# Performance work log

Measured on AMD Instinct MI355X. Metric: run time of the kernel, lower is better.

The kernel has to match this reference:

```python
import jax, jax.numpy as jnp
import numpy as np

N, E, G = 50000, 800000, 128
H, NUM_RBF, CUTOFF, TIME_DIM, L = 128, 32, 6.0, 64, 4
MAX_Z, LIGAND_NODE = 128, 1
M_IN = 3 * H + NUM_RBF + 1


def _ln(x, g, b, eps=1e-5):
    mu = x.mean(-1, keepdims=True)
    var = ((x - mu) ** 2).mean(-1, keepdims=True)
    return (x - mu) * jax.lax.rsqrt(var + eps) * g + b


def _sin_emb(t, dim):
    half = dim // 2
    freqs = jnp.exp(jnp.arange(half, dtype=jnp.float32) * (-np.log(10000.0) / (half - 1)))
    args = t[:, None] * freqs[None, :]
    return jnp.concatenate([jnp.sin(args), jnp.cos(args)], axis=-1)


def setup_inputs() -> dict:
    key = jax.random.key(0)
    ks = jax.random.split(key, 32)
    d = {}
    d['z'] = jax.random.randint(ks[0], (N,), 0, MAX_Z)
    d['node_type'] = jax.random.randint(ks[1], (N,), 0, 2)
    d['pos'] = jax.random.normal(ks[2], (N, 3), jnp.float32) * 3.0
    d['edge_index'] = jax.random.randint(ks[3], (2, E), 0, N)
    d['edge_type'] = jax.random.randint(ks[4], (E,), 0, 2)
    d['batch'] = jnp.sort(jax.random.randint(ks[5], (N,), 0, G))
    d['t'] = jax.random.uniform(ks[6], (G,), jnp.float32)

    def lin(k, fi, fo):
        return jax.random.normal(k, (fi, fo), jnp.float32) / np.sqrt(fi)

    d['emb_z'] = jax.random.normal(ks[7], (MAX_Z, H), jnp.float32) * 0.02
    d['emb_nt'] = jax.random.normal(ks[8], (2, H), jnp.float32) * 0.02
    d['in_norm_g'] = jnp.ones((H,), jnp.float32)
    d['in_norm_b'] = jnp.zeros((H,), jnp.float32)
    d['time_w1'] = lin(ks[9], TIME_DIM, H); d['time_b1'] = jnp.zeros((H,), jnp.float32)
    d['time_w2'] = lin(ks[10], H, H); d['time_b2'] = jnp.zeros((H,), jnp.float32)
    d['l_edge_emb'] = jax.random.normal(ks[11], (L, 2, H), jnp.float32) * 0.02
    d['l_msg_w1'] = jax.random.normal(ks[12], (L, M_IN, H), jnp.float32) / np.sqrt(M_IN)
    d['l_msg_b1'] = jnp.zeros((L, H), jnp.float32)
    d['l_msg_w2'] = jax.random.normal(ks[13], (L, H, H), jnp.float32) / np.sqrt(H)
    d['l_msg_b2'] = jnp.zeros((L, H), jnp.float32)
    d['l_upd_w1'] = jax.random.normal(ks[14], (L, 2 * H, H), jnp.float32) / np.sqrt(2 * H)
    d['l_upd_b1'] = jnp.zeros((L, H), jnp.float32)
    d['l_upd_w2'] = jax.random.normal(ks[15], (L, H, H), jnp.float32) / np.sqrt(H)
    d['l_upd_b2'] = jnp.zeros((L, H), jnp.float32)
    d['l_norm_g'] = jnp.ones((L, H), jnp.float32)
    d['l_norm_b'] = jnp.zeros((L, H), jnp.float32)
    d['head_w1'] = lin(ks[16], H, H); d['head_b1'] = jnp.zeros((H,), jnp.float32)
    d['head_w2'] = lin(ks[17], H, 1); d['head_b2'] = jnp.zeros((1,), jnp.float32)
    return d


def reference(z, node_type, pos, edge_index, edge_type, batch, t,
              emb_z, emb_nt, in_norm_g, in_norm_b,
              time_w1, time_b1, time_w2, time_b2,
              l_edge_emb, l_msg_w1, l_msg_b1, l_msg_w2, l_msg_b2,
              l_upd_w1, l_upd_b1, l_upd_w2, l_upd_b2, l_norm_g, l_norm_b,
              head_w1, head_b1, head_w2, head_b2):
    centers = jnp.linspace(0.0, CUTOFF, NUM_RBF)
    step = CUTOFF / (NUM_RBF - 1)
    gamma = 1.0 / max(step * step, 1e-6)

    h = emb_z[jnp.clip(z, 0, MAX_Z - 1)] + emb_nt[node_type]
    tf = jax.nn.silu(_sin_emb(t, TIME_DIM) @ time_w1 + time_b1) @ time_w2 + time_b2
    h = h + tf[batch]
    h = _ln(h, in_norm_g, in_norm_b)

    src, dst = edge_index[0], edge_index[1]
    rel = pos[src] - pos[dst]                     # [E,3]
    dist = jnp.linalg.norm(rel, axis=-1)          # [E]
    radial = jnp.exp(-gamma * (dist[:, None] - centers[None, :]) ** 2)  # [E,R]
    lig = node_type == LIGAND_NODE

    for i in range(L):
        ek = l_edge_emb[i][edge_type]             # [E,H]
        m_in = jnp.concatenate([h[src], h[dst], ek, radial, dist[:, None]], axis=-1)
        msg = jax.nn.silu(m_in @ l_msg_w1[i] + l_msg_b1[i])
        msg = jax.nn.silu(msg @ l_msg_w2[i] + l_msg_b2[i])
        sums = jax.ops.segment_sum(msg, dst, num_segments=N)
        cnt = jax.ops.segment_sum(jnp.ones((E,), h.dtype), dst, num_segments=N)
        agg = sums / jnp.clip(cnt, 1.0)[:, None]
        upd = jax.nn.silu(jnp.concatenate([h, agg], axis=-1) @ l_upd_w1[i] + l_upd_b1[i])
        upd = upd @ l_upd_w2[i] + l_upd_b2[i]
        h = jnp.where(lig[:, None], _ln(h + upd, l_norm_g[i], l_norm_b[i]), h)

    mask = lig.astype(h.dtype)
    gsum = jax.ops.segment_sum(h * mask[:, None], batch, num_segments=G)
    gcnt = jax.ops.segment_sum(mask, batch, num_segments=G)
    gf = gsum / jnp.clip(gcnt, 1.0)[:, None]
    out = jax.nn.silu(gf @ head_w1 + head_b1) @ head_w2 + head_b2
    return out.squeeze(-1)
```

## Files before the change

### kernel.cpp

```cpp
#include <hip/hip_runtime.h>
#include <hip/hip_bf16.h>

#define NN 50000
#define EE 800000
#define GG 128
#define HH 128

typedef __bf16 bf16;
typedef __attribute__((ext_vector_type(8))) __bf16 bf16x8;
typedef __attribute__((ext_vector_type(4))) float f32x4;

__device__ __forceinline__ float silu_f(float x) { return x / (1.0f + __expf(-x)); }

__global__ void prep_weights(const float* __restrict__ w1, const float* __restrict__ w2,
                             const float* __restrict__ u1, const float* __restrict__ u2,
                             const float* __restrict__ ee, const float* __restrict__ mb1,
                             bf16* __restrict__ W1abt, bf16* __restrict__ W1rt,
                             bf16* __restrict__ W2t, bf16* __restrict__ U1t,
                             bf16* __restrict__ U2t) {
    int idx = blockIdx.x * 256 + threadIdx.x;
    if (idx < 131072) {
        int l = idx >> 15, rem = idx & 32767;
        int c = rem >> 7, k = rem & 127;
        int krow = k + ((c >= 128) ? 128 : 0);
        W1abt[idx] = (bf16)w1[(size_t)l * 417 * 128 + (size_t)krow * 128 + (c & 127)];
    } else if ((idx -= 131072) < 32768) {
        int l = idx >> 13, rem = idx & 8191;
        int c = rem >> 6, k = rem & 63;
        const float* w1l = w1 + (size_t)l * 417 * 128;
        float v = 0.0f;
        if (k < 32) v = w1l[(size_t)(384 + k) * 128 + c];
        else if (k == 32) v = w1l[(size_t)416 * 128 + c];
        else if (k == 33) {
            v = mb1[l * 128 + c];
            for (int t = 0; t < 128; ++t)
                v += ee[(size_t)l * 256 + t] * w1l[(size_t)(256 + t) * 128 + c];
        } else if (k == 34) {
            for (int t = 0; t < 128; ++t)
                v += (ee[(size_t)l * 256 + 128 + t] - ee[(size_t)l * 256 + t]) *
                     w1l[(size_t)(256 + t) * 128 + c];
        }
        W1rt[idx] = (bf16)v;
    } else if ((idx -= 32768) < 65536) {
        int l = idx / 16384, rem = idx % 16384;
        int n = rem / 128, k = rem % 128;
        W2t[idx] = (bf16)w2[(size_t)l * 16384 + (size_t)k * 128 + n];
    } else if ((idx -= 65536) < 131072) {
        int l = idx / 32768, rem = idx % 32768;
        int n = rem / 256, k = rem % 256;
        U1t[idx] = (bf16)u1[(size_t)l * 32768 + (size_t)k * 128 + n];
    } else if ((idx -= 131072) < 65536) {
        int l = idx / 16384, rem = idx % 16384;
        int n = rem / 128, k = rem % 128;
        U2t[idx] = (bf16)u2[(size_t)l * 16384 + (size_t)k * 128 + n];
    }
}

__global__ void time_mlp(const float* __restrict__ t, const float* __restrict__ w1,
                         const float* __restrict__ b1, const float* __restrict__ w2,
                         const float* __restrict__ b2, float* __restrict__ tf) {
    int g = blockIdx.x, c = threadIdx.x;
    __shared__ float sL[64], uT[128];
    float tv = t[g];
    if (c < 32) {
        float fr = expf(-(float)c * (logf(10000.0f) / 31.0f));
        float arg = tv * fr;
        sL[c] = sinf(arg);
        sL[c + 32] = cosf(arg);
    }
    __syncthreads();
    float acc = b1[c];
    for (int k = 0; k < 64; ++k) acc += sL[k] * w1[k * 128 + c];
    uT[c] = silu_f(acc);
    __syncthreads();
    float acc2 = b2[c];
    for (int k = 0; k < 128; ++k) acc2 += uT[k] * w2[k * 128 + c];
    tf[g * 128 + c] = acc2;
}

__global__ void node_init(const int* __restrict__ z, const int* __restrict__ nt,
                          const int* __restrict__ batch, const float* __restrict__ tf,
                          const float* __restrict__ emb_z, const float* __restrict__ emb_nt,
                          const float* __restrict__ g, const float* __restrict__ b,
                          float* __restrict__ hg, bf16* __restrict__ hb) {
    int n = blockIdx.x, c = threadIdx.x;
    __shared__ float red[128];
    int zz = min(max(z[n], 0), 127);
    float v = emb_z[zz * 128 + c] + emb_nt[nt[n] * 128 + c] + tf[batch[n] * 128 + c];
    red[c] = v;
    __syncthreads();
    for (int s = 64; s > 0; s >>= 1) { if (c < s) red[c] += red[c + s]; __syncthreads(); }
    float mu = red[0] * (1.0f / 128.0f);
    __syncthreads();
    float dv = v - mu;
    red[c] = dv * dv;
    __syncthreads();
    for (int s = 64; s > 0; s >>= 1) { if (c < s) red[c] += red[c + s]; __syncthreads(); }
    float var = red[0] * (1.0f / 128.0f);
    float o = dv * rsqrtf(var + 1e-5f) * g[c] + b[c];
    hg[(size_t)n * 128 + c] = o;
    hb[(size_t)n * 128 + c] = (bf16)o;
}

__global__ void edge_pre(const int* __restrict__ ei, const float* __restrict__ pos,
                         float* __restrict__ dist_raw, int* __restrict__ cnt) {
    int e = blockIdx.x * 256 + threadIdx.x;
    if (e >= EE) return;
    int s = ei[e], d = ei[EE + e];
    float dx = pos[s * 3 + 0] - pos[d * 3 + 0];
    float dy = pos[s * 3 + 1] - pos[d * 3 + 1];
    float dz = pos[s * 3 + 2] - pos[d * 3 + 2];
    dist_raw[e] = sqrtf(dx * dx + dy * dy + dz * dz);
    atomicAdd(&cnt[d], 1);
}

__global__ void scan_kernel(const int* __restrict__ cnt, int* __restrict__ cursor) {
    __shared__ int part[1024];
    int t = threadIdx.x;
    const int per = (NN + 1023) / 1024;
    int start = t * per, end = min(start + per, NN);
    int s = 0;
    for (int i = start; i < end; ++i) s += cnt[i];
    part[t] = s;
    __syncthreads();
    for (int off = 1; off < 1024; off <<= 1) {
        int v = (t >= off) ? part[t - off] : 0;
        __syncthreads();
        part[t] += v;
        __syncthreads();
    }
    int base = (t == 0) ? 0 : part[t - 1];
    for (int i = start; i < end; ++i) { cursor[i] = base; base += cnt[i]; }
}

__global__ void scatter_kernel(const int* __restrict__ ei, const int* __restrict__ et,
                               const float* __restrict__ dist_raw, int* __restrict__ cursor,
                               int* __restrict__ src_s, int* __restrict__ dst_s,
                               int* __restrict__ type_s, float* __restrict__ dist_s) {
    int e = blockIdx.x * 256 + threadIdx.x;
    if (e >= EE) return;
    int d = ei[EE + e];
    int p = atomicAdd(&cursor[d], 1);
    src_s[p] = ei[e];
    dst_s[p] = d;
    type_s[p] = et[e];
    dist_s[p] = dist_raw[e];
}

__global__ __launch_bounds__(256) void node_pre(
    const bf16* __restrict__ hb, const bf16* __restrict__ W1abt,
    float* __restrict__ Xs, float* __restrict__ Xd) {
    __shared__ bf16 xL[64 * 128];
    const int tid = threadIdx.x;
    const int lane = tid & 63, wave = tid >> 6;
    const int wr = wave >> 1, wc = wave & 1;
    const int lrow = lane & 15, lgrp = lane >> 4;
    const int nb0 = blockIdx.x * 64;
    const int r0 = wr * 32 + lrow, r1 = r0 + 16;

    for (int i = tid; i < 64 * 16; i += 256) {
        const int row = i >> 4, cc = i & 15;
        const int node = nb0 + row;
        bf16x8 v;
        if (node < NN) v = *(const bf16x8*)(hb + (size_t)node * 128 + cc * 8);
        else { for (int j = 0; j < 8; ++j) v[j] = (bf16)0.0f; }
        *(bf16x8*)(xL + row * 128 + ((cc ^ (row & 15)) * 8)) = v;
    }
    __syncthreads();

    f32x4 acc[2][8] = {};
    for (int ks = 0; ks < 4; ++ks) {
        const int cb = ks * 4 + lgrp;
        bf16x8 a0 = *(const bf16x8*)(xL + r0 * 128 + ((cb ^ (r0 & 15)) * 8));
        bf16x8 a1 = *(const bf16x8*)(xL + r1 * 128 + ((cb ^ (r1 & 15)) * 8));
        const int k0 = ks * 32 + lgrp * 8;
#pragma unroll
        for (int ni = 0; ni < 8; ++ni) {
            const int col = wc * 128 + ni * 16 + lrow;
            bf16x8 b = *(const bf16x8*)(W1abt + (size_t)col * 128 + k0);
            acc[0][ni] = __builtin_amdgcn_mfma_f32_16x16x32_bf16(a0, b, acc[0][ni], 0, 0, 0);
            acc[1][ni] = __builtin_amdgcn_mfma_f32_16x16x32_bf16(a1, b, acc[1][ni], 0, 0, 0);
        }
    }
#pragma unroll
    for (int mi = 0; mi < 2; ++mi) {
#pragma unroll
        for (int r = 0; r < 4; ++r) {
            const int row = wr * 32 + mi * 16 + lgrp * 4 + r;
            const int node = nb0 + row;
            if (node >= NN) continue;
#pragma unroll
            for (int ni = 0; ni < 8; ++ni) {
                const int col = wc * 128 + ni * 16 + lrow;
                float v = (mi == 0 ? acc[0][ni][r] : acc[1][ni][r]);
                if (col < 128) Xs[(size_t)node * 128 + col] = v;
                else Xd[(size_t)node * 128 + (col - 128)] = v;
            }
        }
    }
}

__global__ __launch_bounds__(256) void edge_kernel(
    const int* __restrict__ src_s, const int* __restrict__ dst_s,
    const int* __restrict__ type_s, const float* __restrict__ dist_s,
    const float* __restrict__ Xs, const float* __restrict__ Xd,
    const bf16* __restrict__ W1rt, const bf16* __restrict__ W2t,
    const float* __restrict__ b2, float* __restrict__ sums) {
    __shared__ bf16 msgL[64 * 128];
    __shared__ int dstL[64];
    __shared__ int srcL[64];
    const int tid = threadIdx.x;
    const int lane = tid & 63, wave = tid >> 6;
    const int wr = wave >> 1, wc = wave & 1;
    const int lrow = lane & 15, lgrp = lane >> 4;
    const int eb = blockIdx.x * 64;

    const int r0 = wr * 32 + lrow;
    const int r1 = r0 + 16;
    const int e0 = eb + r0, e1 = eb + r1;
    const int ty0 = type_s[e0], ty1 = type_s[e1];
    const float di0 = dist_s[e0], di1 = dist_s[e1];
    if (tid < 64) { dstL[tid] = dst_s[eb + tid]; srcL[tid] = src_s[eb + tid]; }
    __syncthreads();

    const float step = 6.0f / 31.0f;
    const float gamma = 1.0f / (step * step);

    f32x4 acc[2][4] = {};
#pragma unroll
    for (int ks = 0; ks < 2; ++ks) {
        const int k0 = ks * 32 + lgrp * 8;
        bf16x8 a0, a1;
        if (k0 < 32) {
#pragma unroll
            for (int j = 0; j < 8; ++j) {
                float cj = (float)(k0 + j) * step;
                float v0 = di0 - cj, v1 = di1 - cj;
                a0[j] = (bf16)__expf(-gamma * v0 * v0);
                a1[j] = (bf16)__expf(-gamma * v1 * v1);
            }
        } else {
#pragma unroll
            for (int j = 0; j < 8; ++j) { a0[j] = (bf16)0.0f; a1[j] = (bf16)0.0f; }
            if (k0 == 32) {
                a0[0] = (bf16)di0; a1[0] = (bf16)di1;
                a0[1] = (bf16)1.0f; a1[1] = (bf16)1.0f;
                a0[2] = (bf16)(float)ty0; a1[2] = (bf16)(float)ty1;
            }
        }
#pragma unroll
        for (int ni = 0; ni < 4; ++ni) {
            const int col = wc * 64 + ni * 16 + lrow;
            bf16x8 b = *(const bf16x8*)(W1rt + (size_t)col * 64 + k0);
            acc[0][ni] = __builtin_amdgcn_mfma_f32_16x16x32_bf16(a0, b, acc[0][ni], 0, 0, 0);
            acc[1][ni] = __builtin_amdgcn_mfma_f32_16x16x32_bf16(a1, b, acc[1][ni], 0, 0, 0);
        }
    }
#pragma unroll
    for (int mi = 0; mi < 2; ++mi) {
#pragma unroll
        for (int r = 0; r < 4; ++r) {
            const int row = wr * 32 + mi * 16 + lgrp * 4 + r;
            const int sn = srcL[row], dn = dstL[row];
            const float* xs = Xs + (size_t)sn * 128;
            const float* xd = Xd + (size_t)dn * 128;
#pragma unroll
            for (int ni = 0; ni < 4; ++ni) {
                const int col = wc * 64 + ni * 16 + lrow;
                float v = (mi == 0 ? acc[0][ni][r] : acc[1][ni][r]) + xs[col] + xd[col];
                v = silu_f(v);
                const int cc = col >> 3;
                msgL[row * 128 + ((cc ^ (row & 15)) * 8) + (col & 7)] = (bf16)v;
            }
        }
    }
    __syncthreads();

    f32x4 acc2[2][4] = {};
#pragma unroll
    for (int ks = 0; ks < 4; ++ks) {
        const int cb = ks * 4 + lgrp;
        bf16x8 a0 = *(const bf16x8*)(msgL + r0 * 128 + ((cb ^ (r0 & 15)) * 8));
        bf16x8 a1 = *(const bf16x8*)(msgL + r1 * 128 + ((cb ^ (r1 & 15)) * 8));
        const int k0 = ks * 32 + lgrp * 8;
#pragma unroll
        for (int ni = 0; ni < 4; ++ni) {
            const int col = wc * 64 + ni * 16 + lrow;
            bf16x8 b = *(const bf16x8*)(W2t + (size_t)col * 128 + k0);
            acc2[0][ni] = __builtin_amdgcn_mfma_f32_16x16x32_bf16(a0, b, acc2[0][ni], 0, 0, 0);
            acc2[1][ni] = __builtin_amdgcn_mfma_f32_16x16x32_bf16(a1, b, acc2[1][ni], 0, 0, 0);
        }
    }
    __syncthreads();
#pragma unroll
    for (int mi = 0; mi < 2; ++mi) {
#pragma unroll
        for (int ni = 0; ni < 4; ++ni) {
            const int col = wc * 64 + ni * 16 + lrow;
            const float bias = b2[col];
            const int cc = col >> 3;
#pragma unroll
            for (int r = 0; r < 4; ++r) {
                const int row = wr * 32 + mi * 16 + lgrp * 4 + r;
                float v = silu_f((mi == 0 ? acc2[0][ni][r] : acc2[1][ni][r]) + bias);
                msgL[row * 128 + ((cc ^ (row & 15)) * 8) + (col & 7)] = (bf16)v;
            }
        }
    }
    __syncthreads();
    {
        const int cp = (tid & 63) * 2;
        const int q = tid >> 6;
        const int cc = cp >> 3;
        float a0s = 0.0f, a1s = 0.0f;
        int cur = dstL[q * 16];
        for (int i = 0; i < 16; ++i) {
            const int row = q * 16 + i;
            const int dd = dstL[row];
            if (dd != cur) {
                atomicAdd(&sums[(size_t)cur * 128 + cp], a0s);
                atomicAdd(&sums[(size_t)cur * 128 + cp + 1], a1s);
                a0s = 0.0f; a1s = 0.0f; cur = dd;
            }
            const int off = row * 128 + ((cc ^ (row & 15)) * 8) + (cp & 7);
            a0s += (float)msgL[off];
            a1s += (float)msgL[off + 1];
        }
        atomicAdd(&sums[(size_t)cur * 128 + cp], a0s);
        atomicAdd(&sums[(size_t)cur * 128 + cp + 1], a1s);
    }
}

__global__ __launch_bounds__(256) void node_kernel(
    float* __restrict__ hg, bf16* __restrict__ hb, const float* __restrict__ sums,
    const int* __restrict__ cnt, const int* __restrict__ node_type,
    const bf16* __restrict__ U1t, const bf16* __restrict__ U2t,
    const float* __restrict__ ub1, const float* __restrict__ ub2,
    const float* __restrict__ ng, const float* __restrict__ nb_) {
    __shared__ char smem[49152];
    bf16* xL = (bf16*)smem;
    bf16* uL = (bf16*)(smem + 32768);
    float* u2f = (float*)smem;
    const int tid = threadIdx.x;
    const int lane = tid & 63, wave = tid >> 6;
    const int wr = wave >> 1, wc = wave & 1;
    const int lrow = lane & 15, lgrp = lane >> 4;
    const int nb0 = blockIdx.x * 64;
    const int r0 = wr * 32 + lrow, r1 = r0 + 16;

    for (int i = tid; i < 64 * 32; i += 256) {
        const int row = i >> 5, cc = i & 31;
        const int node = nb0 + row;
        bf16x8 v;
        if (node < NN) {
            const int col8 = cc * 8;
            if (col8 < 128) {
                v = *(const bf16x8*)(hb + (size_t)node * 128 + col8);
            } else {
                const float inv = 1.0f / fmaxf((float)cnt[node], 1.0f);
                const float4 f0 = *(const float4*)(sums + (size_t)node * 128 + (col8 - 128));
                const float4 f1 = *(const float4*)(sums + (size_t)node * 128 + (col8 - 128) + 4);
                v[0] = (bf16)(f0.x * inv); v[1] = (bf16)(f0.y * inv);
                v[2] = (bf16)(f0.z * inv); v[3] = (bf16)(f0.w * inv);
                v[4] = (bf16)(f1.x * inv); v[5] = (bf16)(f1.y * inv);
                v[6] = (bf16)(f1.z * inv); v[7] = (bf16)(f1.w * inv);
            }
        } else {
#pragma unroll
            for (int j = 0; j < 8; ++j) v[j] = (bf16)0.0f;
        }
        *(bf16x8*)(xL + row * 256 + ((cc ^ (row & 15)) * 8)) = v;
    }
    __syncthreads();

    f32x4 acc[2][4] = {};
    for (int ks = 0; ks < 8; ++ks) {
        const int cb = ks * 4 + lgrp;
        bf16x8 a0 = *(const bf16x8*)(xL + r0 * 256 + ((cb ^ (r0 & 15)) * 8));
        bf16x8 a1 = *(const bf16x8*)(xL + r1 * 256 + ((cb ^ (r1 & 15)) * 8));
        const int k0 = ks * 32 + lgrp * 8;
#pragma unroll
        for (int ni = 0; ni < 4; ++ni) {
            const int col = wc * 64 + ni * 16 + lrow;
            bf16x8 b = *(const bf16x8*)(U1t + (size_t)col * 256 + k0);
            acc[0][ni] = __builtin_amdgcn_mfma_f32_16x16x32_bf16(a0, b, acc[0][ni], 0, 0, 0);
            acc[1][ni] = __builtin_amdgcn_mfma_f32_16x16x32_bf16(a1, b, acc[1][ni], 0, 0, 0);
        }
    }
#pragma unroll
    for (int mi = 0; mi < 2; ++mi) {
#pragma unroll
        for (int ni = 0; ni < 4; ++ni) {
            const int col = wc * 64 + ni * 16 + lrow;
            const float bias = ub1[col];
            const int cc = col >> 3;
#pragma unroll
            for (int r = 0; r < 4; ++r) {
                const int row = wr * 32 + mi * 16 + lgrp * 4 + r;
                float v = silu_f((mi == 0 ? acc[0][ni][r] : acc[1][ni][r]) + bias);
                uL[row * 128 + ((cc ^ (row & 15)) * 8) + (col & 7)] = (bf16)v;
            }
        }
    }
    __syncthreads();

    f32x4 acc2[2][4] = {};
    for (int ks = 0; ks < 4; ++ks) {
        const int cb = ks * 4 + lgrp;
        bf16x8 a0 = *(const bf16x8*)(uL + r0 * 128 + ((cb ^ (r0 & 15)) * 8));
        bf16x8 a1 = *(const bf16x8*)(uL + r1 * 128 + ((cb ^ (r1 & 15)) * 8));
        const int k0 = ks * 32 + lgrp * 8;
#pragma unroll
        for (int ni = 0; ni < 4; ++ni) {
            const int col = wc * 64 + ni * 16 + lrow;
            bf16x8 b = *(const bf16x8*)(U2t + (size_t)col * 128 + k0);
            acc2[0][ni] = __builtin_amdgcn_mfma_f32_16x16x32_bf16(a0, b, acc2[0][ni], 0, 0, 0);
            acc2[1][ni] = __builtin_amdgcn_mfma_f32_16x16x32_bf16(a1, b, acc2[1][ni], 0, 0, 0);
        }
    }
    __syncthreads();
#pragma unroll
    for (int mi = 0; mi < 2; ++mi) {
#pragma unroll
        for (int ni = 0; ni < 4; ++ni) {
            const int col = wc * 64 + ni * 16 + lrow;
            const float bias = ub2[col];
#pragma unroll
            for (int r = 0; r < 4; ++r) {
                const int row = wr * 32 + mi * 16 + lgrp * 4 + r;
                u2f[row * 129 + col] = (mi == 0 ? acc2[0][ni][r] : acc2[1][ni][r]) + bias;
            }
        }
    }
    __syncthreads();
    if (tid < 64) {
        const int node = nb0 + tid;
        if (node < NN && node_type[node] == 1) {
            float sum = 0.0f, sq = 0.0f;
            for (int c = 0; c < 128; ++c) {
                float s = hg[(size_t)node * 128 + c] + u2f[tid * 129 + c];
                sum += s; sq += s * s;
            }
            float mu = sum * (1.0f / 128.0f);
            float var = sq * (1.0f / 128.0f) - mu * mu;
            float rstd = rsqrtf(var + 1e-5f);
            for (int c = 0; c < 128; ++c) {
                float s = hg[(size_t)node * 128 + c] + u2f[tid * 129 + c];
                float o = (s - mu) * rstd * ng[c] + nb_[c];
                hg[(size_t)node * 128 + c] = o;
                hb[(size_t)node * 128 + c] = (bf16)o;
            }
        }
    }
}

__global__ void pool_kernel(const int* __restrict__ nt, const int* __restrict__ batch,
                            const float* __restrict__ hg, float* __restrict__ gsum,
                            float* __restrict__ gcnt) {
    int idx = blockIdx.x * 256 + threadIdx.x;
    int n = idx >> 7, c = idx & 127;
    if (n >= NN) return;
    if (nt[n] == 1) {
        int b = batch[n];
        atomicAdd(&gsum[b * 128 + c], hg[(size_t)n * 128 + c]);
        if (c == 0) atomicAdd(&gcnt[b], 1.0f);
    }
}

__global__ void head_kernel(const float* __restrict__ gsum, const float* __restrict__ gcnt,
                            const float* __restrict__ w1, const float* __restrict__ b1,
                            const float* __restrict__ w2, const float* __restrict__ b2,
                            float* __restrict__ out) {
    int g = blockIdx.x, c = threadIdx.x;
    __shared__ float gfL[128], uH[128];
    float inv = 1.0f / fmaxf(gcnt[g], 1.0f);
    gfL[c] = gsum[g * 128 + c] * inv;
    __syncthreads();
    float acc = b1[c];
    for (int k = 0; k < 128; ++k) acc += gfL[k] * w1[k * 128 + c];
    uH[c] = silu_f(acc);
    __syncthreads();
    gfL[c] = uH[c] * w2[c];
    __syncthreads();
    for (int s = 64; s > 0; s >>= 1) { if (c < s) gfL[c] += gfL[c + s]; __syncthreads(); }
    if (c == 0) out[g] = gfL[0] + b2[0];
}

extern "C" void kernel_launch(void* const* d_in, const int* in_sizes, int n_in,
                              void* d_out, int out_size, void* d_ws, size_t ws_size,
                              hipStream_t stream) {
    const int* z = (const int*)d_in[0];
    const int* node_type = (const int*)d_in[1];
    const float* pos = (const float*)d_in[2];
    const int* edge_index = (const int*)d_in[3];
    const int* edge_type = (const int*)d_in[4];
    const int* batch = (const int*)d_in[5];
    const float* t_in = (const float*)d_in[6];
    const float* emb_z = (const float*)d_in[7];
    const float* emb_nt = (const float*)d_in[8];
    const float* in_norm_g = (const float*)d_in[9];
    const float* in_norm_b = (const float*)d_in[10];
    const float* time_w1 = (const float*)d_in[11];
    const float* time_b1 = (const float*)d_in[12];
    const float* time_w2 = (const float*)d_in[13];
    const float* time_b2 = (const float*)d_in[14];
    const float* l_edge_emb = (const float*)d_in[15];
    const float* l_msg_w1 = (const float*)d_in[16];
    const float* l_msg_b1 = (const float*)d_in[17];
    const float* l_msg_w2 = (const float*)d_in[18];
    const float* l_msg_b2 = (const float*)d_in[19];
    const float* l_upd_w1 = (const float*)d_in[20];
    const float* l_upd_b1 = (const float*)d_in[21];
    const float* l_upd_w2 = (const float*)d_in[22];
    const float* l_upd_b2 = (const float*)d_in[23];
    const float* l_norm_g = (const float*)d_in[24];
    const float* l_norm_b = (const float*)d_in[25];
    const float* head_w1 = (const float*)d_in[26];
    const float* head_b1 = (const float*)d_in[27];
    const float* head_w2 = (const float*)d_in[28];
    const float* head_b2 = (const float*)d_in[29];
    float* out = (float*)d_out;

    char* w = (char*)d_ws;
    auto alloc = [&](size_t bytes) {
        char* p = w;
        w += (bytes + 255) & ~(size_t)255;
        return p;
    };
    float* hg = (float*)alloc((size_t)NN * 128 * 4);
    bf16* hb = (bf16*)alloc((size_t)NN * 128 * 2);
    float* sums = (float*)alloc((size_t)NN * 128 * 4);
    float* Xs = (float*)alloc((size_t)NN * 128 * 4);
    float* Xd = (float*)alloc((size_t)NN * 128 * 4);
    int* cnt = (int*)alloc((size_t)NN * 4);
    int* cursor = (int*)alloc((size_t)NN * 4);
    int* src_s = (int*)alloc((size_t)EE * 4);
    int* dst_s = (int*)alloc((size_t)EE * 4);
    int* type_s = (int*)alloc((size_t)EE * 4);
    float* dist_s = (float*)alloc((size_t)EE * 4);
    float* dist_raw = (float*)alloc((size_t)EE * 4);
    bf16* W1abt = (bf16*)alloc((size_t)4 * 256 * 128 * 2);
    bf16* W1rt = (bf16*)alloc((size_t)4 * 128 * 64 * 2);
    bf16* W2t = (bf16*)alloc((size_t)4 * 128 * 128 * 2);
    bf16* U1t = (bf16*)alloc((size_t)4 * 128 * 256 * 2);
    bf16* U2t = (bf16*)alloc((size_t)4 * 128 * 128 * 2);
    float* tf = (float*)alloc((size_t)GG * 128 * 4);
    float* gsum = (float*)alloc((size_t)GG * 128 * 4);
    float* gcnt = (float*)alloc((size_t)GG * 4);

    hipMemsetAsync(cnt, 0, (size_t)NN * 4, stream);
    prep_weights<<<1664, 256, 0, stream>>>(l_msg_w1, l_msg_w2, l_upd_w1, l_upd_w2,
                                           l_edge_emb, l_msg_b1, W1abt, W1rt, W2t, U1t, U2t);
    time_mlp<<<GG, 128, 0, stream>>>(t_in, time_w1, time_b1, time_w2, time_b2, tf);
    node_init<<<NN, 128, 0, stream>>>(z, node_type, batch, tf, emb_z, emb_nt,
                                      in_norm_g, in_norm_b, hg, hb);
    edge_pre<<<(EE + 255) / 256, 256, 0, stream>>>(edge_index, pos, dist_raw, cnt);
    scan_kernel<<<1, 1024, 0, stream>>>(cnt, cursor);
    scatter_kernel<<<(EE + 255) / 256, 256, 0, stream>>>(edge_index, edge_type, dist_raw,
                                                         cursor, src_s, dst_s, type_s, dist_s);
    for (int l = 0; l < 4; ++l) {
        node_pre<<<(NN + 63) / 64, 256, 0, stream>>>(hb, W1abt + (size_t)l * 32768, Xs, Xd);
        hipMemsetAsync(sums, 0, (size_t)NN * 128 * 4, stream);
        edge_kernel<<<EE / 64, 256, 0, stream>>>(
            src_s, dst_s, type_s, dist_s, Xs, Xd, W1rt + (size_t)l * 8192,
            W2t + (size_t)l * 16384, l_msg_b2 + l * 128, sums);
        node_kernel<<<(NN + 63) / 64, 256, 0, stream>>>(
            hg, hb, sums, cnt, node_type, U1t + (size_t)l * 32768, U2t + (size_t)l * 16384,
            l_upd_b1 + l * 128, l_upd_b2 + l * 128, l_norm_g + l * 128, l_norm_b + l * 128);
    }
    hipMemsetAsync(gsum, 0, (size_t)GG * 128 * 4, stream);
    hipMemsetAsync(gcnt, 0, (size_t)GG * 4, stream);
    pool_kernel<<<(NN * 128 + 255) / 256, 256, 0, stream>>>(node_type, batch, hg, gsum, gcnt);
    head_kernel<<<GG, 128, 0, stream>>>(gsum, gcnt, head_w1, head_b1, head_w2, head_b2, out);
}
```

Measured before the change: 1.504 ms.

## Store per-node message projections in bf16 and stage gathered sums in LDS

node_pre now writes the source and destination projections as bf16, which halves the bytes gathered per edge. The edge kernel uses coalesced 16-byte vector loads to gather both rows, adds them, and stages the sum in a padded LDS buffer instead of doing scalar fp32 gathers inside the MFMA epilogue. The same padded buffer is reused for the second-layer output and read as packed bf16 pairs during the segmented reduction, which also removes one barrier. The cost is extra rounding, since the projections and their sum are now bf16, plus more shared memory per block, which may lower occupancy.

```diff
diff --git a/kernel.cpp b/kernel.cpp
--- a/kernel.cpp
+++ b/kernel.cpp
@@ -5,6 +5,7 @@
 #define EE 800000
 #define GG 128
 #define HH 128
+#define XPB 136
 
 typedef __bf16 bf16;
 typedef __attribute__((ext_vector_type(8))) __bf16 bf16x8;
@@ -149,7 +150,7 @@
 
 __global__ __launch_bounds__(256) void node_pre(
     const bf16* __restrict__ hb, const bf16* __restrict__ W1abt,
-    float* __restrict__ Xs, float* __restrict__ Xd) {
+    bf16* __restrict__ Xsb, bf16* __restrict__ Xdb) {
     __shared__ bf16 xL[64 * 128];
     const int tid = threadIdx.x;
     const int lane = tid & 63, wave = tid >> 6;
@@ -193,8 +194,8 @@
             for (int ni = 0; ni < 8; ++ni) {
                 const int col = wc * 128 + ni * 16 + lrow;
                 float v = (mi == 0 ? acc[0][ni][r] : acc[1][ni][r]);
-                if (col < 128) Xs[(size_t)node * 128 + col] = v;
-                else Xd[(size_t)node * 128 + (col - 128)] = v;
+                if (col < 128) Xsb[(size_t)node * 128 + col] = (bf16)v;
+                else Xdb[(size_t)node * 128 + (col - 128)] = (bf16)v;
             }
         }
     }
@@ -203,9 +204,10 @@
 __global__ __launch_bounds__(256) void edge_kernel(
     const int* __restrict__ src_s, const int* __restrict__ dst_s,
     const int* __restrict__ type_s, const float* __restrict__ dist_s,
-    const float* __restrict__ Xs, const float* __restrict__ Xd,
+    const bf16* __restrict__ Xsb, const bf16* __restrict__ Xdb,
     const bf16* __restrict__ W1rt, const bf16* __restrict__ W2t,
     const float* __restrict__ b2, float* __restrict__ sums) {
+    __shared__ bf16 xbL[64 * XPB];
     __shared__ bf16 msgL[64 * 128];
     __shared__ int dstL[64];
     __shared__ int srcL[64];
@@ -223,6 +225,17 @@
     if (tid < 64) { dstL[tid] = dst_s[eb + tid]; srcL[tid] = src_s[eb + tid]; }
     __syncthreads();
 
+#pragma unroll
+    for (int i = tid; i < 64 * 16; i += 256) {
+        const int row = i >> 4, c8 = (i & 15) << 3;
+        bf16x8 a = *(const bf16x8*)(Xsb + (size_t)srcL[row] * 128 + c8);
+        bf16x8 b = *(const bf16x8*)(Xdb + (size_t)dstL[row] * 128 + c8);
+        bf16x8 s;
+#pragma unroll
+        for (int j = 0; j < 8; ++j) s[j] = (bf16)((float)a[j] + (float)b[j]);
+        *(bf16x8*)(xbL + row * XPB + c8) = s;
+    }
+
     const float step = 6.0f / 31.0f;
     const float gamma = 1.0f / (step * step);
 
@@ -256,18 +269,18 @@
             acc[1][ni] = __builtin_amdgcn_mfma_f32_16x16x32_bf16(a1, b, acc[1][ni], 0, 0, 0);
         }
     }
+    __syncthreads();
+
 #pragma unroll
     for (int mi = 0; mi < 2; ++mi) {
 #pragma unroll
         for (int r = 0; r < 4; ++r) {
             const int row = wr * 32 + mi * 16 + lgrp * 4 + r;
-            const int sn = srcL[row], dn = dstL[row];
-            const float* xs = Xs + (size_t)sn * 128;
-            const float* xd = Xd + (size_t)dn * 128;
+            const bf16* xr = xbL + row * XPB;
 #pragma unroll
             for (int ni = 0; ni < 4; ++ni) {
                 const int col = wc * 64 + ni * 16 + lrow;
-                float v = (mi == 0 ? acc[0][ni][r] : acc[1][ni][r]) + xs[col] + xd[col];
+                float v = (mi == 0 ? acc[0][ni][r] : acc[1][ni][r]) + (float)xr[col];
                 v = silu_f(v);
                 const int cc = col >> 3;
                 msgL[row * 128 + ((cc ^ (row & 15)) * 8) + (col & 7)] = (bf16)v;
@@ -291,19 +304,17 @@
             acc2[1][ni] = __builtin_amdgcn_mfma_f32_16x16x32_bf16(a1, b, acc2[1][ni], 0, 0, 0);
         }
     }
-    __syncthreads();
 #pragma unroll
     for (int mi = 0; mi < 2; ++mi) {
 #pragma unroll
         for (int ni = 0; ni < 4; ++ni) {
             const int col = wc * 64 + ni * 16 + lrow;
             const float bias = b2[col];
-            const int cc = col >> 3;
 #pragma unroll
             for (int r = 0; r < 4; ++r) {
                 const int row = wr * 32 + mi * 16 + lgrp * 4 + r;
                 float v = silu_f((mi == 0 ? acc2[0][ni][r] : acc2[1][ni][r]) + bias);
-                msgL[row * 128 + ((cc ^ (row & 15)) * 8) + (col & 7)] = (bf16)v;
+                xbL[row * XPB + col] = (bf16)v;
             }
         }
     }
@@ -311,7 +322,6 @@
     {
         const int cp = (tid & 63) * 2;
         const int q = tid >> 6;
-        const int cc = cp >> 3;
         float a0s = 0.0f, a1s = 0.0f;
         int cur = dstL[q * 16];
         for (int i = 0; i < 16; ++i) {
@@ -322,9 +332,9 @@
                 atomicAdd(&sums[(size_t)cur * 128 + cp + 1], a1s);
                 a0s = 0.0f; a1s = 0.0f; cur = dd;
             }
-            const int off = row * 128 + ((cc ^ (row & 15)) * 8) + (cp & 7);
-            a0s += (float)msgL[off];
-            a1s += (float)msgL[off + 1];
+            const unsigned u = *(const unsigned*)(xbL + row * XPB + cp);
+            a0s += __uint_as_float(u << 16);
+            a1s += __uint_as_float(u & 0xffff0000u);
         }
         atomicAdd(&sums[(size_t)cur * 128 + cp], a0s);
         atomicAdd(&sums[(size_t)cur * 128 + cp + 1], a1s);
@@ -530,8 +540,8 @@
     float* hg = (float*)alloc((size_t)NN * 128 * 4);
     bf16* hb = (bf16*)alloc((size_t)NN * 128 * 2);
     float* sums = (float*)alloc((size_t)NN * 128 * 4);
-    float* Xs = (float*)alloc((size_t)NN * 128 * 4);
-    float* Xd = (float*)alloc((size_t)NN * 128 * 4);
+    bf16* Xsb = (bf16*)alloc((size_t)NN * 128 * 2);
+    bf16* Xdb = (bf16*)alloc((size_t)NN * 128 * 2);
     int* cnt = (int*)alloc((size_t)NN * 4);
     int* cursor = (int*)alloc((size_t)NN * 4);
     int* src_s = (int*)alloc((size_t)EE * 4);
@@ -559,10 +569,10 @@
     scatter_kernel<<<(EE + 255) / 256, 256, 0, stream>>>(edge_index, edge_type, dist_raw,
                                                          cursor, src_s, dst_s, type_s, dist_s);
     for (int l = 0; l < 4; ++l) {
-        node_pre<<<(NN + 63) / 64, 256, 0, stream>>>(hb, W1abt + (size_t)l * 32768, Xs, Xd);
+        node_pre<<<(NN + 63) / 64, 256, 0, stream>>>(hb, W1abt + (size_t)l * 32768, Xsb, Xdb);
         hipMemsetAsync(sums, 0, (size_t)NN * 128 * 4, stream);
         edge_kernel<<<EE / 64, 256, 0, stream>>>(
-            src_s, dst_s, type_s, dist_s, Xs, Xd, W1rt + (size_t)l * 8192,
+            src_s, dst_s, type_s, dist_s, Xsb, Xdb, W1rt + (size_t)l * 8192,
             W2t + (size_t)l * 16384, l_msg_b2 + l * 128, sums);
         node_kernel<<<(NN + 63) / 64, 256, 0, stream>>>(
             hg, hb, sums, cnt, node_type, U1t + (size_t)l * 32768, U2t + (size_t)l * 16384,
```

After: 1.456 ms. 3.2% less time.
